# Kernel optimization log

Hardware: AMD Instinct MI355X
Metric: run time of the kernel (lower is better)

The kernel has to match this reference:

```python
import jax, jax.numpy as jnp
import numpy as np

B, N = 2, 2048
TOP_K = 48
NUM_RBF = 16
MAX_REL = 32            # max_relative_feature
NUM_POS = 16            # num_positional_embeddings
EDGE_FEATURES = 128
EDGE_IN = NUM_POS + NUM_RBF * 25  # 416
POS_IN = 2 * MAX_REL + 2          # 66 one-hot classes


def setup_inputs() -> dict:
    key = jax.random.key(0)
    k0, k1, k2, k3 = jax.random.split(key, 4)
    X = jax.random.normal(k0, (B, N, 4, 3), dtype=jnp.float32) * 3.0
    mask = jnp.ones((B, N), dtype=jnp.float32)
    R_idx = jnp.arange(B * N, dtype=jnp.int32).reshape(B, N)
    chain_labels = jax.random.randint(k1, (B, N), 0, 4).astype(jnp.int32)
    W_pos = 0.05 * jax.random.normal(k2, (POS_IN, NUM_POS), dtype=jnp.float32)
    b_pos = jnp.zeros((NUM_POS,), dtype=jnp.float32)
    W_edge = 0.05 * jax.random.normal(k3, (EDGE_IN, EDGE_FEATURES), dtype=jnp.float32)
    b_edge = jnp.zeros((EDGE_FEATURES,), dtype=jnp.float32)
    return {"X": X, "mask": mask, "R_idx": R_idx, "chain_labels": chain_labels,
            "W_pos": W_pos, "b_pos": b_pos, "W_edge": W_edge, "b_edge": b_edge}


def _rbf(D):
    # D: [..., K] -> [..., K, NUM_RBF]
    mu = jnp.linspace(2.0, 22.0, NUM_RBF)        # D_min=2, D_max=22
    sigma = (22.0 - 2.0) / NUM_RBF               # 1.25
    return jnp.exp(-(((D[..., None] - mu) / sigma) ** 2))


def _pair_dist(A, Bc):
    # A, Bc: [B, N, 3] -> [B, N, N]
    return jnp.sqrt(jnp.sum((A[:, :, None, :] - Bc[:, None, :, :]) ** 2, axis=-1) + 1e-6)


def reference(X, mask, R_idx, chain_labels, W_pos, b_pos, W_edge, b_edge):
    # virtual Cbeta from backbone geometry
    b = X[:, :, 1, :] - X[:, :, 0, :]
    c = X[:, :, 2, :] - X[:, :, 1, :]
    a = jnp.cross(b, c, axis=-1)
    Cb = -0.58273431 * a + 0.56802827 * b - 0.54067466 * c + X[:, :, 1, :]
    Ca, Nat, Cat, Oat = X[:, :, 1, :], X[:, :, 0, :], X[:, :, 2, :], X[:, :, 3, :]

    # masked Ca-Ca distances + k nearest neighbors
    mask2 = mask[:, None, :] * mask[:, :, None]
    D = mask2 * _pair_dist(Ca, Ca)
    D_adjust = D + (1.0 - mask2) * jnp.max(D, axis=-1, keepdims=True)
    neg_D, E_idx = jax.lax.top_k(-D_adjust, min(TOP_K, N))  # smallest distances
    D_neighbors = -neg_D                                     # [B, N, K]

    rbfs = [_rbf(D_neighbors)]
    pairs = [(Nat, Nat), (Cat, Cat), (Oat, Oat), (Cb, Cb),
             (Ca, Nat), (Ca, Cat), (Ca, Oat), (Ca, Cb),
             (Nat, Cat), (Nat, Oat), (Nat, Cb), (Cb, Cat), (Cb, Oat), (Oat, Cat),
             (Nat, Ca), (Cat, Ca), (Oat, Ca), (Cb, Ca),
             (Cat, Nat), (Oat, Nat), (Cb, Nat), (Cat, Cb), (Oat, Cb), (Cat, Oat)]
    for A_, B_ in pairs:  # fixed structural set of 24 atom-pair types
        Dab = _pair_dist(A_, B_)                          # [B, N, N]
        Dn = jnp.take_along_axis(Dab, E_idx, axis=2)      # [B, N, K]
        rbfs.append(_rbf(Dn))
    RBF_all = jnp.concatenate(rbfs, axis=-1)              # [B, N, K, 25*NUM_RBF]

    # relative positional / chain features at the gathered neighbors
    offset = R_idx[:, :, None] - R_idx[:, None, :]
    offset = jnp.take_along_axis(offset, E_idx, axis=2)   # [B, N, K]
    d_chains = (chain_labels[:, :, None] == chain_labels[:, None, :]).astype(jnp.int32)
    E_chains = jnp.take_along_axis(d_chains, E_idx, axis=2)

    d = jnp.clip(offset + MAX_REL, 0, 2 * MAX_REL)
    d = d * E_chains + (1 - E_chains) * (2 * MAX_REL + 1)
    d_onehot = jax.nn.one_hot(d, POS_IN, dtype=jnp.float32)  # [B, N, K, 66]
    E_positional = d_onehot @ W_pos + b_pos                  # [B, N, K, 16]

    E = jnp.concatenate((E_positional, RBF_all), axis=-1)    # [B, N, K, 416]
    E = E @ W_edge + b_edge                                  # [B, N, K, 128]
    return E, E_idx
```

## Files before the change

kernel.cpp:

```cpp
#include <hip/hip_runtime.h>
#include <hip/hip_bf16.h>
#include <stdint.h>

#define BB   2
#define NN   2048
#define BN   (BB*NN)
#define KTOP 48
#define EIN  416
#define EF   128

typedef __attribute__((ext_vector_type(8))) short s8v;
typedef __attribute__((ext_vector_type(4))) float f32x4;
typedef __attribute__((ext_vector_type(4))) unsigned int u32x4;
typedef unsigned short u16;
typedef unsigned int u32;
typedef unsigned long long u64;

__device__ __constant__ int cPA[25] = {1,0,2,3,4,1,1,1,1,0,0,0,4,4,3,0,2,3,4,2,3,4,2,3,2};
__device__ __constant__ int cPB[25] = {1,0,2,3,4,0,2,3,4,2,3,4,2,3,2,1,1,1,1,0,0,0,4,4,3};

__device__ __forceinline__ u16 bf16u(float x) {
  __hip_bfloat16 h = __float2bfloat16(x);
  return *reinterpret_cast<u16*>(&h);
}
__device__ __forceinline__ u32 pack2(float lo, float hi) {
  return (u32)bf16u(lo) | ((u32)bf16u(hi) << 16);
}

__global__ __launch_bounds__(256) void prep_kernel(const float* __restrict__ X,
                                                   const float* __restrict__ W_edge,
                                                   float* __restrict__ atoms5p,
                                                   float* __restrict__ capack4,
                                                   u16* __restrict__ wtf) {
  int tid = blockIdx.x * 256 + threadIdx.x;
  if (tid < EIN * EF) {
    int k = tid >> 7, n = tid & 127;
    wtf[((size_t)(k >> 3)) * 1024 + n * 8 + (k & 7)] = bf16u(W_edge[tid]);
  } else if (tid < EIN * EF + BN) {
    int idx = tid - EIN * EF;
    const float* x = X + (size_t)idx * 12;
    float Nx = x[0], Ny = x[1], Nz = x[2];
    float Cax = x[3], Cay = x[4], Caz = x[5];
    float Cx = x[6], Cy = x[7], Cz = x[8];
    float Ox = x[9], Oy = x[10], Oz = x[11];
    float bx = Cax - Nx, by = Cay - Ny, bz = Caz - Nz;
    float cx = Cx - Cax, cy = Cy - Cay, cz = Cz - Caz;
    float ax = by * cz - bz * cy;
    float ay = bz * cx - bx * cz;
    float az = bx * cy - by * cx;
    float Cbx = -0.58273431f * ax + 0.56802827f * bx - 0.54067466f * cx + Cax;
    float Cby = -0.58273431f * ay + 0.56802827f * by - 0.54067466f * cy + Cay;
    float Cbz = -0.58273431f * az + 0.56802827f * bz - 0.54067466f * cz + Caz;
    f32x4* o = (f32x4*)(atoms5p + (size_t)idx * 20);
    o[0] = (f32x4){Nx, Ny, Nz, 0.f};
    o[1] = (f32x4){Cax, Cay, Caz, 0.f};
    o[2] = (f32x4){Cx, Cy, Cz, 0.f};
    o[3] = (f32x4){Ox, Oy, Oz, 0.f};
    o[4] = (f32x4){Cbx, Cby, Cbz, 0.f};
    *(f32x4*)(capack4 + (size_t)idx * 4) = (f32x4){Cax, Cay, Caz, 0.f};
  }
}

__device__ __forceinline__ u32 blockExclScan(u32 v, u32* scanw, int t) {
  int lane = t & 63, w = t >> 6;
  u32 inc = v;
#pragma unroll
  for (int off = 1; off < 64; off <<= 1) {
    u32 o = __shfl_up(inc, off);
    if (lane >= off) inc += o;
  }
  if (lane == 63) scanw[w] = inc;
  __syncthreads();
  u32 base = 0;
  for (int ww = 0; ww < w; ++ww) base += scanw[ww];
  __syncthreads();
  return base + inc - v;
}

template<int NB, bool CHKPREF>
__device__ __forceinline__ void radix_round(u32* hist, u32* scanw, u32* selinfo, int t,
                                            const u32* kv, u32 pref, int prefShift,
                                            int binShift, u32 binMask, u32 r) {
  const int PB = NB / 256;
#pragma unroll
  for (int q = 0; q < PB / 4; ++q)
    *(u32x4*)&hist[t * PB + q * 4] = (u32x4){0, 0, 0, 0};
  __syncthreads();
#pragma unroll
  for (int s = 0; s < 8; ++s) {
    bool ok = (!CHKPREF) || ((kv[s] >> prefShift) == pref);
    if (ok) atomicAdd(&hist[(kv[s] >> binShift) & binMask], 1u);
  }
  __syncthreads();
  u32 loc[PB];
  u32 sum = 0;
#pragma unroll
  for (int q = 0; q < PB / 4; ++q) {
    u32x4 lv = *(u32x4*)&hist[t * PB + q * 4];
    loc[q * 4 + 0] = lv.x; loc[q * 4 + 1] = lv.y;
    loc[q * 4 + 2] = lv.z; loc[q * 4 + 3] = lv.w;
    sum += lv.x + lv.y + lv.z + lv.w;
  }
  int lane = t & 63, w = t >> 6;
  u32 inc = sum;
#pragma unroll
  for (int off = 1; off < 64; off <<= 1) {
    u32 o = __shfl_up(inc, off);
    if (lane >= off) inc += o;
  }
  if (lane == 63) scanw[w] = inc;
  __syncthreads();
  u32 base = 0;
  for (int ww = 0; ww < w; ++ww) base += scanw[ww];
  u32 c = base + inc - sum;
#pragma unroll
  for (int q = 0; q < PB; ++q) {
    u32 nc = c + loc[q];
    if (c < r && r <= nc) { selinfo[0] = (u32)(t * PB + q); selinfo[1] = r - c; }
    c = nc;
  }
  __syncthreads();
}

__global__ __launch_bounds__(256) void topk_kernel(const float* __restrict__ capack4,
                                                   const float* __restrict__ mask,
                                                   float* __restrict__ dtop,
                                                   float* __restrict__ eidx_f) {
  __shared__ u32 hist[4096];
  __shared__ u32 scanw[4];
  __shared__ u32 selinfo[2];
  __shared__ float redf[4];
  __shared__ u64 win[64];

  int row = blockIdx.x;
  int b = row >> 11, i = row & (NN - 1);
  int t = threadIdx.x, lane = t & 63, w = t >> 6;
  const float* cab4 = capack4 + (size_t)b * NN * 4;
  const float* mrow = mask + (size_t)b * NN;
  f32x4 ci = *(const f32x4*)&cab4[(size_t)i * 4];
  float mi = mrow[i];
  f32x4 mk0 = *(const f32x4*)&mrow[t * 8];
  f32x4 mk1 = *(const f32x4*)&mrow[t * 8 + 4];

  float dvv[8], m2v[8];
  float lmax = 0.f;
#pragma unroll
  for (int s = 0; s < 8; ++s) {
    f32x4 cj = *(const f32x4*)&cab4[(size_t)(t * 8 + s) * 4];
    float dx = ci.x - cj.x, dy = ci.y - cj.y, dz = ci.z - cj.z;
    float d = sqrtf(dx * dx + dy * dy + dz * dz + 1e-6f);
    float mj = (s < 4) ? mk0[s] : mk1[s - 4];
    float m2 = mi * mj;
    float D = m2 * d;
    dvv[s] = D; m2v[s] = m2;
    lmax = fmaxf(lmax, D);
  }
#pragma unroll
  for (int off = 32; off >= 1; off >>= 1) lmax = fmaxf(lmax, __shfl_xor(lmax, off));
  if (lane == 0) redf[w] = lmax;
  __syncthreads();
  float rmax = fmaxf(fmaxf(redf[0], redf[1]), fmaxf(redf[2], redf[3]));

  u32 kv[8];
#pragma unroll
  for (int s = 0; s < 8; ++s)
    kv[s] = __float_as_uint(dvv[s] + (1.0f - m2v[s]) * rmax);

  u32 r = KTOP;
  radix_round<4096, false>(hist, scanw, selinfo, t, kv, 0, 0, 20, 0xFFFu, r);
  u32 sel1 = selinfo[0]; r = selinfo[1];
  radix_round<1024, true>(hist, scanw, selinfo, t, kv, sel1, 20, 10, 0x3FFu, r);
  u32 sel2 = selinfo[0]; r = selinfo[1];
  u32 pref12 = (sel1 << 10) | sel2;
  radix_round<1024, true>(hist, scanw, selinfo, t, kv, pref12, 10, 0, 0x3FFu, r);
  u32 sel3 = selinfo[0];
  u32 takeEq = selinfo[1];
  u32 T = (sel1 << 20) | (sel2 << 10) | sel3;

  u32 lcnt = 0, ecnt = 0;
#pragma unroll
  for (int s = 0; s < 8; ++s) { lcnt += (kv[s] < T); ecnt += (kv[s] == T); }
  u32 ebase = blockExclScan(ecnt, scanw, t);
  u32 taken = 0;
  if (ebase < takeEq) { u32 room = takeEq - ebase; taken = room < ecnt ? room : ecnt; }
  u32 wbase = blockExclScan(lcnt + taken, scanw, t);
  u32 slot = wbase, tleft = taken;
#pragma unroll
  for (int s = 0; s < 8; ++s) {
    u32 j = (u32)(t * 8 + s);
    if (kv[s] < T) {
      win[slot++] = ((u64)kv[s] << 32) | j;
    } else if (kv[s] == T && tleft) {
      win[slot++] = ((u64)kv[s] << 32) | j;
      tleft--;
    }
  }
  __syncthreads();

  if (w == 0) {
    u64 key = (lane < KTOP) ? win[lane] : ~0ull;
#pragma unroll
    for (int k = 2; k <= 64; k <<= 1) {
#pragma unroll
      for (int jj = k >> 1; jj >= 1; jj >>= 1) {
        u64 p = __shfl_xor(key, jj);
        bool lowerl = (lane & jj) == 0;
        bool asc = (lane & k) == 0;
        u64 mn = p < key ? p : key;
        u64 mx = p < key ? key : p;
        key = (lowerl == asc) ? mn : mx;
      }
    }
    if (lane < KTOP) {
      u32 j = (u32)(key & 0xffffffffu);
      eidx_f[row * KTOP + lane] = (float)j;
      dtop[row * KTOP + lane] = __uint_as_float((u32)(key >> 32));
    }
  }
}

__device__ __forceinline__ s8v rbf8(float D, float mu0) {
  float Dc = fminf(D, 40.0f);
  float t0 = (Dc - mu0) * 0.8f;
  float v0 = __expf(-t0 * t0);
  float g = __expf(fmaf(2.13333333f, t0, -1.13777778f));
  const float C = 0.10273985f;
  float v1 = v0 * g; g *= C;
  float v2 = v1 * g; g *= C;
  float v3 = v2 * g; g *= C;
  float v4 = v3 * g; g *= C;
  float v5 = v4 * g; g *= C;
  float v6 = v5 * g; g *= C;
  float v7 = v6 * g;
  union { u32x4 u; s8v s; } cv;
  cv.u = (u32x4){pack2(v0, v1), pack2(v2, v3), pack2(v4, v5), pack2(v6, v7)};
  return cv.s;
}

__global__ __launch_bounds__(256, 4) void edge_kernel(const float* __restrict__ atoms5p,
                                                      const u16* __restrict__ wtf,
                                                      const float* __restrict__ eidx_f,
                                                      const float* __restrict__ dtop,
                                                      const int* __restrict__ Ridx,
                                                      const int* __restrict__ chains,
                                                      const float* __restrict__ Wpos,
                                                      const float* __restrict__ bpos,
                                                      const float* __restrict__ bedge,
                                                      float* __restrict__ Eout) {
  __shared__ float D_lds[KTOP][29];
  __shared__ u32 pos_lds[KTOP][8];
  __shared__ f32x4 aJ[KTOP][5];
  __shared__ f32x4 aI[5];
  __shared__ int jbuf[KTOP];

  int row = blockIdx.x;
  int b = row >> 11, i = row & (NN - 1);
  int t = threadIdx.x;
  const float* atomsB = atoms5p + (size_t)b * NN * 20;

  if (t < KTOP * 5) {
    int k = t / 5, a = t - k * 5;
    int j = (int)eidx_f[row * KTOP + k];
    aJ[k][a] = *(const f32x4*)&atomsB[(size_t)j * 20 + a * 4];
    if (a == 0) jbuf[k] = j;
  } else if (t < KTOP * 5 + 5) {
    int a = t - KTOP * 5;
    aI[a] = *(const f32x4*)&atomsB[(size_t)i * 20 + a * 4];
  }
  if (t < KTOP) D_lds[t][0] = dtop[row * KTOP + t];
  __syncthreads();

#pragma unroll
  for (int q = 0; q < 5; ++q) {
    int e = t + q * 256;
    if (e < 1152) {
      int k = e / 24;
      int p = e - k * 24 + 1;
      f32x4 I = aI[cPA[p]];
      f32x4 J = aJ[k][cPB[p]];
      float dx = I.x - J.x, dy = I.y - J.y, dz = I.z - J.z;
      D_lds[k][p] = __builtin_amdgcn_sqrtf(dx * dx + dy * dy + dz * dz + 1e-6f);
    } else if (e < 1200) {
      int k = e - 1152;
      int j = jbuf[k];
      int Ri = Ridx[b * NN + i], Rj = Ridx[b * NN + j];
      int same = (chains[b * NN + i] == chains[b * NN + j]);
      int off = Ri - Rj + 32;
      off = off < 0 ? 0 : (off > 64 ? 64 : off);
      int drow = same ? off : 65;
      const float* wr = Wpos + drow * 16;
      u32 pk[8];
#pragma unroll
      for (int h = 0; h < 4; ++h) {
        f32x4 wv = *(const f32x4*)&wr[h * 4];
        f32x4 bv = *(const f32x4*)&bpos[h * 4];
        pk[h * 2 + 0] = pack2(wv.x + bv.x, wv.y + bv.y);
        pk[h * 2 + 1] = pack2(wv.z + bv.z, wv.w + bv.w);
      }
      *(u32x4*)&pos_lds[k][0] = (u32x4){pk[0], pk[1], pk[2], pk[3]};
      *(u32x4*)&pos_lds[k][4] = (u32x4){pk[4], pk[5], pk[6], pk[7]};
    }
  }
  __syncthreads();

  int w = t >> 6, lane = t & 63;
  int lr = lane & 15, lg = lane >> 4;
  int col0 = w * 32 + lr, col1 = col0 + 16;
  const float MU8 = 12.6666667f;
  f32x4 acc[3][2] = {};

  {
    s8v bf0 = *reinterpret_cast<const s8v*>(&wtf[(size_t)lg * 1024 + col0 * 8]);
    s8v bf1 = *reinterpret_cast<const s8v*>(&wtf[(size_t)lg * 1024 + col1 * 8]);
#pragma unroll
    for (int mt = 0; mt < 3; ++mt) {
      int m = mt * 16 + lr;
      s8v af;
      if (lg < 2) {
        af = *reinterpret_cast<const s8v*>(&pos_lds[m][lg * 4]);
      } else {
        af = rbf8(D_lds[m][0], (lg == 2) ? 2.0f : MU8);
      }
      acc[mt][0] = __builtin_amdgcn_mfma_f32_16x16x32_bf16(af, bf0, acc[mt][0], 0, 0, 0);
      acc[mt][1] = __builtin_amdgcn_mfma_f32_16x16x32_bf16(af, bf1, acc[mt][1], 0, 0, 0);
    }
  }
#pragma unroll
  for (int kc = 1; kc < 13; ++kc) {
    int p = 2 * kc - 1 + (lg >> 1);
    float mu0 = (lg & 1) ? MU8 : 2.0f;
    s8v bf0 = *reinterpret_cast<const s8v*>(&wtf[(size_t)(kc * 4 + lg) * 1024 + col0 * 8]);
    s8v bf1 = *reinterpret_cast<const s8v*>(&wtf[(size_t)(kc * 4 + lg) * 1024 + col1 * 8]);
#pragma unroll
    for (int mt = 0; mt < 3; ++mt) {
      s8v af = rbf8(D_lds[mt * 16 + lr][p], mu0);
      acc[mt][0] = __builtin_amdgcn_mfma_f32_16x16x32_bf16(af, bf0, acc[mt][0], 0, 0, 0);
      acc[mt][1] = __builtin_amdgcn_mfma_f32_16x16x32_bf16(af, bf1, acc[mt][1], 0, 0, 0);
    }
  }

  float bias0 = bedge[col0], bias1 = bedge[col1];
  float* orow = Eout + (size_t)row * KTOP * EF;
#pragma unroll
  for (int mt = 0; mt < 3; ++mt) {
#pragma unroll
    for (int qq = 0; qq < 4; ++qq) {
      int m = mt * 16 + lg * 4 + qq;
      orow[m * EF + col0] = acc[mt][0][qq] + bias0;
      orow[m * EF + col1] = acc[mt][1][qq] + bias1;
    }
  }
}

extern "C" void kernel_launch(void* const* d_in, const int* in_sizes, int n_in,
                              void* d_out, int out_size, void* d_ws, size_t ws_size,
                              hipStream_t stream) {
  const float* X = (const float*)d_in[0];
  const float* mask = (const float*)d_in[1];
  const int* Ridx = (const int*)d_in[2];
  const int* chains = (const int*)d_in[3];
  const float* Wpos = (const float*)d_in[4];
  const float* bpos = (const float*)d_in[5];
  const float* Wedge = (const float*)d_in[6];
  const float* bedge = (const float*)d_in[7];

  float* Eout = (float*)d_out;
  float* EidxF = Eout + (size_t)BN * KTOP * EF;

  u16* wtf = (u16*)d_ws;
  float* atoms5p = (float*)((char*)d_ws + 53248 * 2);
  float* capack4 = atoms5p + (size_t)BN * 20;
  float* dtop = capack4 + (size_t)BN * 4;

  prep_kernel<<<(EIN * EF + BN + 255) / 256, 256, 0, stream>>>(X, Wedge, atoms5p, capack4, wtf);
  topk_kernel<<<BN, 256, 0, stream>>>(capack4, mask, dtop, EidxF);
  edge_kernel<<<BN, 256, 0, stream>>>(atoms5p, wtf, EidxF, dtop, Ridx, chains, Wpos, bpos, bedge, Eout);
}
```

Baseline: 104.2 us.

## Use single-wave edge blocks computing all 128 columns per wave

The edge kernel now runs one 64-thread wave per output row instead of four waves that each owned 32 output columns. The wave computes every RBF A-fragment once and reuses it across all 8 column tiles, where before each of the four waves recomputed the same RBF exponentials. The __syncthreads barriers are removed, atom J coordinates are read straight from global memory, and bf16 packing uses the hardware v_cvt_pk_bf16_f32 instruction. In exchange the kernel needs 24 accumulator tiles per thread, which raises register pressure and may lower occupancy.

```diff
diff --git a/kernel.cpp b/kernel.cpp
--- a/kernel.cpp
+++ b/kernel.cpp
@@ -25,6 +25,11 @@
 }
 __device__ __forceinline__ u32 pack2(float lo, float hi) {
   return (u32)bf16u(lo) | ((u32)bf16u(hi) << 16);
+}
+__device__ __forceinline__ u32 cvtpk(float lo, float hi) {
+  u32 r;
+  asm("v_cvt_pk_bf16_f32 %0, %1, %2" : "=v"(r) : "v"(lo), "v"(hi));
+  return r;
 }
 
 __global__ __launch_bounds__(256) void prep_kernel(const float* __restrict__ X,
@@ -233,121 +238,119 @@
   float v6 = v5 * g; g *= C;
   float v7 = v6 * g;
   union { u32x4 u; s8v s; } cv;
-  cv.u = (u32x4){pack2(v0, v1), pack2(v2, v3), pack2(v4, v5), pack2(v6, v7)};
+  cv.u = (u32x4){cvtpk(v0, v1), cvtpk(v2, v3), cvtpk(v4, v5), cvtpk(v6, v7)};
   return cv.s;
 }
 
-__global__ __launch_bounds__(256, 4) void edge_kernel(const float* __restrict__ atoms5p,
-                                                      const u16* __restrict__ wtf,
-                                                      const float* __restrict__ eidx_f,
-                                                      const float* __restrict__ dtop,
-                                                      const int* __restrict__ Ridx,
-                                                      const int* __restrict__ chains,
-                                                      const float* __restrict__ Wpos,
-                                                      const float* __restrict__ bpos,
-                                                      const float* __restrict__ bedge,
-                                                      float* __restrict__ Eout) {
-  __shared__ float D_lds[KTOP][29];
+__global__ __launch_bounds__(64) void edge_kernel(const float* __restrict__ atoms5p,
+                                                  const u16* __restrict__ wtf,
+                                                  const float* __restrict__ eidx_f,
+                                                  const float* __restrict__ dtop,
+                                                  const int* __restrict__ Ridx,
+                                                  const int* __restrict__ chains,
+                                                  const float* __restrict__ Wpos,
+                                                  const float* __restrict__ bpos,
+                                                  const float* __restrict__ bedge,
+                                                  float* __restrict__ Eout) {
+  __shared__ float D_lds[KTOP][26];
   __shared__ u32 pos_lds[KTOP][8];
-  __shared__ f32x4 aJ[KTOP][5];
-  __shared__ f32x4 aI[5];
   __shared__ int jbuf[KTOP];
-
+  __shared__ f32x4 aI_lds[5];
+
+  int lane = threadIdx.x;
   int row = blockIdx.x;
   int b = row >> 11, i = row & (NN - 1);
-  int t = threadIdx.x;
   const float* atomsB = atoms5p + (size_t)b * NN * 20;
 
-  if (t < KTOP * 5) {
-    int k = t / 5, a = t - k * 5;
-    int j = (int)eidx_f[row * KTOP + k];
-    aJ[k][a] = *(const f32x4*)&atomsB[(size_t)j * 20 + a * 4];
-    if (a == 0) jbuf[k] = j;
-  } else if (t < KTOP * 5 + 5) {
-    int a = t - KTOP * 5;
-    aI[a] = *(const f32x4*)&atomsB[(size_t)i * 20 + a * 4];
-  }
-  if (t < KTOP) D_lds[t][0] = dtop[row * KTOP + t];
-  __syncthreads();
-
-#pragma unroll
-  for (int q = 0; q < 5; ++q) {
-    int e = t + q * 256;
-    if (e < 1152) {
-      int k = e / 24;
-      int p = e - k * 24 + 1;
-      f32x4 I = aI[cPA[p]];
-      f32x4 J = aJ[k][cPB[p]];
-      float dx = I.x - J.x, dy = I.y - J.y, dz = I.z - J.z;
-      D_lds[k][p] = __builtin_amdgcn_sqrtf(dx * dx + dy * dy + dz * dz + 1e-6f);
-    } else if (e < 1200) {
-      int k = e - 1152;
-      int j = jbuf[k];
-      int Ri = Ridx[b * NN + i], Rj = Ridx[b * NN + j];
-      int same = (chains[b * NN + i] == chains[b * NN + j]);
-      int off = Ri - Rj + 32;
-      off = off < 0 ? 0 : (off > 64 ? 64 : off);
-      int drow = same ? off : 65;
-      const float* wr = Wpos + drow * 16;
-      u32 pk[8];
-#pragma unroll
-      for (int h = 0; h < 4; ++h) {
-        f32x4 wv = *(const f32x4*)&wr[h * 4];
-        f32x4 bv = *(const f32x4*)&bpos[h * 4];
-        pk[h * 2 + 0] = pack2(wv.x + bv.x, wv.y + bv.y);
-        pk[h * 2 + 1] = pack2(wv.z + bv.z, wv.w + bv.w);
-      }
-      *(u32x4*)&pos_lds[k][0] = (u32x4){pk[0], pk[1], pk[2], pk[3]};
-      *(u32x4*)&pos_lds[k][4] = (u32x4){pk[4], pk[5], pk[6], pk[7]};
-    }
-  }
-  __syncthreads();
-
-  int w = t >> 6, lane = t & 63;
+  if (lane < 5) aI_lds[lane] = *(const f32x4*)&atomsB[(size_t)i * 20 + lane * 4];
+  if (lane < KTOP) {
+    int j = (int)eidx_f[(size_t)row * KTOP + lane];
+    jbuf[lane] = j;
+    D_lds[lane][0] = dtop[(size_t)row * KTOP + lane];
+    int Ri = Ridx[b * NN + i], Rj = Ridx[b * NN + j];
+    int same = (chains[b * NN + i] == chains[b * NN + j]);
+    int off = Ri - Rj + 32;
+    off = off < 0 ? 0 : (off > 64 ? 64 : off);
+    int drow = same ? off : 65;
+    const float* wr = Wpos + drow * 16;
+    u32 pk[8];
+#pragma unroll
+    for (int h = 0; h < 4; ++h) {
+      f32x4 wv = *(const f32x4*)&wr[h * 4];
+      f32x4 bv = *(const f32x4*)&bpos[h * 4];
+      pk[h * 2 + 0] = cvtpk(wv.x + bv.x, wv.y + bv.y);
+      pk[h * 2 + 1] = cvtpk(wv.z + bv.z, wv.w + bv.w);
+    }
+    *(u32x4*)&pos_lds[lane][0] = (u32x4){pk[0], pk[1], pk[2], pk[3]};
+    *(u32x4*)&pos_lds[lane][4] = (u32x4){pk[4], pk[5], pk[6], pk[7]};
+  }
+
+#pragma unroll
+  for (int q = 0; q < 18; ++q) {
+    int e = q * 64 + lane;
+    int k = e / 24;
+    int p = e - k * 24 + 1;
+    int j = jbuf[k];
+    f32x4 I = aI_lds[cPA[p]];
+    f32x4 J = *(const f32x4*)&atomsB[(size_t)j * 20 + cPB[p] * 4];
+    float dx = I.x - J.x, dy = I.y - J.y, dz = I.z - J.z;
+    D_lds[k][p] = __builtin_amdgcn_sqrtf(dx * dx + dy * dy + dz * dz + 1e-6f);
+  }
+
   int lr = lane & 15, lg = lane >> 4;
-  int col0 = w * 32 + lr, col1 = col0 + 16;
+  const u16* wk = wtf + (size_t)lg * 1024 + lr * 8;
   const float MU8 = 12.6666667f;
-  f32x4 acc[3][2] = {};
+  f32x4 acc[3][8] = {};
 
   {
-    s8v bf0 = *reinterpret_cast<const s8v*>(&wtf[(size_t)lg * 1024 + col0 * 8]);
-    s8v bf1 = *reinterpret_cast<const s8v*>(&wtf[(size_t)lg * 1024 + col1 * 8]);
-#pragma unroll
-    for (int mt = 0; mt < 3; ++mt) {
-      int m = mt * 16 + lr;
-      s8v af;
-      if (lg < 2) {
-        af = *reinterpret_cast<const s8v*>(&pos_lds[m][lg * 4]);
-      } else {
-        af = rbf8(D_lds[m][0], (lg == 2) ? 2.0f : MU8);
-      }
-      acc[mt][0] = __builtin_amdgcn_mfma_f32_16x16x32_bf16(af, bf0, acc[mt][0], 0, 0, 0);
-      acc[mt][1] = __builtin_amdgcn_mfma_f32_16x16x32_bf16(af, bf1, acc[mt][1], 0, 0, 0);
+    s8v a0, a1, a2;
+    if (lg < 2) {
+      a0 = *reinterpret_cast<const s8v*>(&pos_lds[lr][lg * 4]);
+      a1 = *reinterpret_cast<const s8v*>(&pos_lds[16 + lr][lg * 4]);
+      a2 = *reinterpret_cast<const s8v*>(&pos_lds[32 + lr][lg * 4]);
+    } else {
+      float mu0 = (lg == 2) ? 2.0f : MU8;
+      a0 = rbf8(D_lds[lr][0], mu0);
+      a1 = rbf8(D_lds[16 + lr][0], mu0);
+      a2 = rbf8(D_lds[32 + lr][0], mu0);
+    }
+#pragma unroll
+    for (int nt = 0; nt < 8; ++nt) {
+      s8v bv = *reinterpret_cast<const s8v*>(wk + nt * 128);
+      acc[0][nt] = __builtin_amdgcn_mfma_f32_16x16x32_bf16(a0, bv, acc[0][nt], 0, 0, 0);
+      acc[1][nt] = __builtin_amdgcn_mfma_f32_16x16x32_bf16(a1, bv, acc[1][nt], 0, 0, 0);
+      acc[2][nt] = __builtin_amdgcn_mfma_f32_16x16x32_bf16(a2, bv, acc[2][nt], 0, 0, 0);
     }
   }
 #pragma unroll
   for (int kc = 1; kc < 13; ++kc) {
     int p = 2 * kc - 1 + (lg >> 1);
     float mu0 = (lg & 1) ? MU8 : 2.0f;
-    s8v bf0 = *reinterpret_cast<const s8v*>(&wtf[(size_t)(kc * 4 + lg) * 1024 + col0 * 8]);
-    s8v bf1 = *reinterpret_cast<const s8v*>(&wtf[(size_t)(kc * 4 + lg) * 1024 + col1 * 8]);
-#pragma unroll
-    for (int mt = 0; mt < 3; ++mt) {
-      s8v af = rbf8(D_lds[mt * 16 + lr][p], mu0);
-      acc[mt][0] = __builtin_amdgcn_mfma_f32_16x16x32_bf16(af, bf0, acc[mt][0], 0, 0, 0);
-      acc[mt][1] = __builtin_amdgcn_mfma_f32_16x16x32_bf16(af, bf1, acc[mt][1], 0, 0, 0);
-    }
-  }
-
-  float bias0 = bedge[col0], bias1 = bedge[col1];
+    s8v a0 = rbf8(D_lds[lr][p], mu0);
+    s8v a1 = rbf8(D_lds[16 + lr][p], mu0);
+    s8v a2 = rbf8(D_lds[32 + lr][p], mu0);
+    const u16* wkc = wk + (size_t)kc * 4096;
+#pragma unroll
+    for (int nt = 0; nt < 8; ++nt) {
+      s8v bv = *reinterpret_cast<const s8v*>(wkc + nt * 128);
+      acc[0][nt] = __builtin_amdgcn_mfma_f32_16x16x32_bf16(a0, bv, acc[0][nt], 0, 0, 0);
+      acc[1][nt] = __builtin_amdgcn_mfma_f32_16x16x32_bf16(a1, bv, acc[1][nt], 0, 0, 0);
+      acc[2][nt] = __builtin_amdgcn_mfma_f32_16x16x32_bf16(a2, bv, acc[2][nt], 0, 0, 0);
+    }
+  }
+
+  float bias[8];
+#pragma unroll
+  for (int nt = 0; nt < 8; ++nt) bias[nt] = bedge[nt * 16 + lr];
   float* orow = Eout + (size_t)row * KTOP * EF;
 #pragma unroll
   for (int mt = 0; mt < 3; ++mt) {
 #pragma unroll
     for (int qq = 0; qq < 4; ++qq) {
-      int m = mt * 16 + lg * 4 + qq;
-      orow[m * EF + col0] = acc[mt][0][qq] + bias0;
-      orow[m * EF + col1] = acc[mt][1][qq] + bias1;
+      float* pr = orow + (size_t)(mt * 16 + lg * 4 + qq) * EF + lr;
+#pragma unroll
+      for (int nt = 0; nt < 8; ++nt)
+        pr[nt * 16] = acc[mt][nt][qq] + bias[nt];
     }
   }
 }
@@ -374,5 +377,5 @@
 
   prep_kernel<<<(EIN * EF + BN + 255) / 256, 256, 0, stream>>>(X, Wedge, atoms5p, capack4, wtf);
   topk_kernel<<<BN, 256, 0, stream>>>(capack4, mask, dtop, EidxF);
-  edge_kernel<<<BN, 256, 0, stream>>>(atoms5p, wtf, EidxF, dtop, Ridx, chains, Wpos, bpos, bedge, Eout);
-}
+  edge_kernel<<<BN, 64, 0, stream>>>(atoms5p, wtf, EidxF, dtop, Ridx, chains, Wpos, bpos, bedge, Eout);
+}
```

Measured after the change: 92.72 us. -11.0%, faster.
